# Optimization experiments

Hardware: AMD Instinct MI355X
Metric: run time of the kernel (lower is better)

Reference implementation:

```python
import jax, jax.numpy as jnp
import numpy as np

HEADS = 4
KD = 32          # key_dim per head
LEVELS = 2
G = 3            # 2**dims - 1 HP orientation groups
STRENGTH = 0.25
DECAY = 0.6
LN_EPS = 1e-5
MIX_EPS = 1e-3


def _layernorm(x, g, b):
    m = jnp.mean(x, axis=-1, keepdims=True)
    v = jnp.var(x, axis=-1, keepdims=True)
    return (x - m) * jax.lax.rsqrt(v + LN_EPS) * g + b


def _dwt2(x):
    # Haar analysis, periodic/even sizes. [B,H,W,C] -> [B,H/2,W/2,4C] (LL,LH,HL,HH)
    x00 = x[:, 0::2, 0::2]; x01 = x[:, 0::2, 1::2]
    x10 = x[:, 1::2, 0::2]; x11 = x[:, 1::2, 1::2]
    ll = (x00 + x01 + x10 + x11) * 0.5
    lh = (x00 - x01 + x10 - x11) * 0.5
    hl = (x00 + x01 - x10 - x11) * 0.5
    hh = (x00 - x01 - x10 + x11) * 0.5
    return jnp.concatenate([ll, lh, hl, hh], axis=-1)


def _idwt2(w):
    # exact Haar synthesis: [B,H/2,W/2,4C] -> [B,H,W,C]
    ll, lh, hl, hh = jnp.split(w, 4, axis=-1)
    x00 = (ll + lh + hl + hh) * 0.5
    x01 = (ll - lh + hl - hh) * 0.5
    x10 = (ll + lh - hl - hh) * 0.5
    x11 = (ll - lh - hl + hh) * 0.5
    B, H2, W2, C = ll.shape
    r0 = jnp.stack([x00, x01], axis=3).reshape(B, H2, 2 * W2, C)  # interleave W
    r1 = jnp.stack([x10, x11], axis=3).reshape(B, H2, 2 * W2, C)
    return jnp.stack([r0, r1], axis=2).reshape(B, 2 * H2, 2 * W2, C)  # interleave H


def _axial_mhsa(x, p):
    # AxialMHSAND: sequential sweep over spatial axes; each pass is
    # proj(attn(softmax(QK^T/sqrt(d)) V)) on norm(x), qkv via 1x1 conv (=matmul).
    g, b, wq, bq, wk, bk, wv, bv, wp, bp = p
    scale = KD ** -0.5
    for axis in (1, 2):
        X = _layernorm(x, g, b)
        B, H, W, _ = X.shape
        Q = (X @ wq + bq).reshape(B, H, W, HEADS, KD)
        K = (X @ wk + bk).reshape(B, H, W, HEADS, KD)
        V = (X @ wv + bv).reshape(B, H, W, HEADS, KD)
        if axis == 1:  # attend along H, batch over (B, W, heads)
            A = jax.nn.softmax(jnp.einsum('bqwnd,bkwnd->bwnqk', Q, K) * scale, axis=-1)
            Y = jnp.einsum('bwnqk,bkwnd->bqwnd', A, V)
        else:          # attend along W, batch over (B, H, heads)
            A = jax.nn.softmax(jnp.einsum('bhqnd,bhknd->bhnqk', Q, K) * scale, axis=-1)
            Y = jnp.einsum('bhnqk,bhknd->bhqnd', A, V)
        x = Y.reshape(B, H, W, HEADS * KD) @ wp + bp
    return x


def setup_inputs() -> dict:
    key = jax.random.key(0)
    ks = jax.random.split(key, 24)
    C = 64
    HD = HEADS * KD
    s = 0.02
    inp = {'x': jax.random.normal(ks[0], (4, 256, 256, C), jnp.float32)}
    i = 1
    for pre in ('lp', 'hp'):
        inp[pre + '_ln_g'] = jnp.ones((C,), jnp.float32)
        inp[pre + '_ln_b'] = jnp.zeros((C,), jnp.float32)
        inp[pre + '_wq'] = jax.random.normal(ks[i], (C, HD), jnp.float32) * s
        inp[pre + '_bq'] = jax.random.normal(ks[i + 1], (HD,), jnp.float32) * s
        inp[pre + '_wk'] = jax.random.normal(ks[i + 2], (C, HD), jnp.float32) * s
        inp[pre + '_bk'] = jax.random.normal(ks[i + 3], (HD,), jnp.float32) * s
        inp[pre + '_wv'] = jax.random.normal(ks[i + 4], (C, HD), jnp.float32) * s
        inp[pre + '_bv'] = jax.random.normal(ks[i + 5], (HD,), jnp.float32) * s
        inp[pre + '_wp'] = jax.random.normal(ks[i + 6], (HD, C), jnp.float32) * s
        inp[pre + '_bp'] = jax.random.normal(ks[i + 7], (C,), jnp.float32) * s
        i += 8
    mix = jnp.eye(G, dtype=jnp.float32) + MIX_EPS * (jnp.ones((G, G), jnp.float32) - jnp.eye(G, dtype=jnp.float32))
    inp['mix_w0'] = mix
    inp['mix_w1'] = mix
    return inp


def reference(x, lp_ln_g, lp_ln_b, lp_wq, lp_bq, lp_wk, lp_bk, lp_wv, lp_bv, lp_wp, lp_bp,
              hp_ln_g, hp_ln_b, hp_wq, hp_bq, hp_wk, hp_bk, hp_wv, hp_bv, hp_wp, hp_bp,
              mix_w0, mix_w1):
    lp_p = (lp_ln_g, lp_ln_b, lp_wq, lp_bq, lp_wk, lp_bk, lp_wv, lp_bv, lp_wp, lp_bp)
    hp_p = (hp_ln_g, hp_ln_b, hp_wq, hp_bq, hp_wk, hp_bk, hp_wv, hp_bv, hp_wp, hp_bp)
    mix_ws = [mix_w0, mix_w1]
    C = x.shape[-1]
    cur = x
    hps = []
    for _ in range(LEVELS):  # analysis pyramid
        w = _dwt2(cur)
        hps.append(w[..., C:])
        cur = w[..., :C]
    # deepest LP: axial attention, residual with full strength
    cur = cur + STRENGTH * _axial_mhsa(cur, lp_p)
    for l in reversed(range(LEVELS)):  # synthesis with per-level HP processing
        hp = hps[l]
        B, H2, W2, _ = hp.shape
        gain = STRENGTH * (DECAY ** (LEVELS - 1 - l))  # coarser levels stronger
        hp_g = hp.reshape(B, H2, W2, G, C)
        mixed = jnp.einsum('gd,bhwdc->bhwgc', mix_ws[l], hp_g)  # OrientationMix
        batched = mixed.transpose(3, 0, 1, 2, 4).reshape(G * B, H2, W2, C)
        att = _axial_mhsa(batched, hp_p)  # shared hp_attn across groups/levels
        att = att.reshape(G, B, H2, W2, C).transpose(1, 2, 3, 0, 4).reshape(B, H2, W2, G * C)
        hp_out = hp + gain * att
        cur = _idwt2(jnp.concatenate([cur, hp_out], axis=-1))
    return cur
```

## Files before the change

kernel.cpp:

```cpp
#include <hip/hip_runtime.h>

#define LN_EPS 1e-5f
#define QSCALE 0.25500526578425445f

typedef __attribute__((ext_vector_type(8))) short bf16x8;
typedef __attribute__((ext_vector_type(4))) float f32x4;

#define MFMA16(A, B, C) __builtin_amdgcn_mfma_f32_16x16x32_bf16(A, B, C, 0, 0, 0)

static __device__ __forceinline__ unsigned short f2bf_rne(float f) {
    union { unsigned int i; float f; } c; c.f = f;
    unsigned int i = c.i;
    return (unsigned short)((i + 0x7fffu + ((i >> 16) & 1u)) >> 16);
}
static __device__ __forceinline__ void bfstore2(unsigned short* p, float x, float y) {
    *(unsigned int*)p = (unsigned int)f2bf_rne(x) | ((unsigned int)f2bf_rne(y) << 16);
}
static __device__ __forceinline__ unsigned pk2(float a, float b) {
    return __builtin_amdgcn_perm(__builtin_bit_cast(unsigned, b),
                                 __builtin_bit_cast(unsigned, a), 0x07060302u);
}
static __device__ __forceinline__ unsigned short tb16(float f) {
    return (unsigned short)(__builtin_bit_cast(unsigned, f) >> 16);
}

__global__ void dwt_kernel(const float4* __restrict__ in, float4* __restrict__ ll,
                           float4* __restrict__ hp, int B, int H2, int W2) {
    const int i = blockIdx.x * blockDim.x + threadIdx.x;
    const int total = B * H2 * W2 * 16;
    if (i >= total) return;
    const int c4 = i & 15;
    int t = i >> 4;
    const int w2 = t % W2; t /= W2;
    const int h2 = t % H2;
    const int b = t / H2;
    const int W = W2 * 2;
    const size_t base = (((size_t)b * (H2 * 2) + 2 * h2) * W + 2 * w2) * 16 + c4;
    const float4 x00 = in[base];
    const float4 x01 = in[base + 16];
    const float4 x10 = in[base + (size_t)W * 16];
    const float4 x11 = in[base + (size_t)W * 16 + 16];
    float4 vll, vlh, vhl, vhh;
#define DWTC(a) \
    vll.a = (x00.a + x01.a + x10.a + x11.a) * 0.5f; \
    vlh.a = (x00.a - x01.a + x10.a - x11.a) * 0.5f; \
    vhl.a = (x00.a + x01.a - x10.a - x11.a) * 0.5f; \
    vhh.a = (x00.a - x01.a - x10.a + x11.a) * 0.5f;
    DWTC(x) DWTC(y) DWTC(z) DWTC(w)
#undef DWTC
    const size_t oi = ((size_t)b * H2 + h2) * W2 + w2;
    ll[oi * 16 + c4] = vll;
    hp[oi * 48 + c4] = vlh;
    hp[oi * 48 + 16 + c4] = vhl;
    hp[oi * 48 + 32 + c4] = vhh;
}

__global__ void idwt_kernel(const float4* __restrict__ cur, const float4* __restrict__ hp,
                            const float4* __restrict__ att, float gain,
                            float4* __restrict__ out, int B, int H2, int W2) {
    const int i = blockIdx.x * blockDim.x + threadIdx.x;
    const int total = B * H2 * W2 * 16;
    if (i >= total) return;
    const int c4 = i & 15;
    int t = i >> 4;
    const int w2 = t % W2; t /= W2;
    const int h2 = t % H2;
    const int b = t / H2;
    const size_t oi = ((size_t)b * H2 + h2) * W2 + w2;
    const size_t sp = (size_t)h2 * W2 + w2;
    const size_t gstr = (size_t)B * H2 * W2;
    const float4 vll = cur[oi * 16 + c4];
    float4 vlh = hp[oi * 48 + c4];
    float4 vhl = hp[oi * 48 + 16 + c4];
    float4 vhh = hp[oi * 48 + 32 + c4];
    const float4 a0 = att[((size_t)b * H2 * W2 + sp) * 16 + c4];
    const float4 a1 = att[((size_t)b * H2 * W2 + gstr + sp) * 16 + c4];
    const float4 a2 = att[((size_t)b * H2 * W2 + 2 * gstr + sp) * 16 + c4];
#define ADDG(a) \
    vlh.a = fmaf(gain, a0.a, vlh.a); \
    vhl.a = fmaf(gain, a1.a, vhl.a); \
    vhh.a = fmaf(gain, a2.a, vhh.a);
    ADDG(x) ADDG(y) ADDG(z) ADDG(w)
#undef ADDG
    float4 x00, x01, x10, x11;
#define IDWTC(a) \
    x00.a = (vll.a + vlh.a + vhl.a + vhh.a) * 0.5f; \
    x01.a = (vll.a - vlh.a + vhl.a - vhh.a) * 0.5f; \
    x10.a = (vll.a + vlh.a - vhl.a - vhh.a) * 0.5f; \
    x11.a = (vll.a - vlh.a - vhl.a + vhh.a) * 0.5f;
    IDWTC(x) IDWTC(y) IDWTC(z) IDWTC(w)
#undef IDWTC
    const int W = W2 * 2;
    const size_t r0 = (((size_t)b * (H2 * 2) + 2 * h2) * W + 2 * w2) * 16 + c4;
    out[r0] = x00;
    out[r0 + 16] = x01;
    out[r0 + (size_t)W * 16] = x10;
    out[r0 + (size_t)W * 16 + 16] = x11;
}

__global__ void prep_weights(const float* __restrict__ lwq, const float* __restrict__ lwk,
                             const float* __restrict__ lwv, const float* __restrict__ lwp,
                             const float* __restrict__ hwq, const float* __restrict__ hwk,
                             const float* __restrict__ hwv, const float* __restrict__ hwp,
                             unsigned short* __restrict__ wbuf) {
    const int i = blockIdx.x * blockDim.x + threadIdx.x;
    if (i >= 65536) return;
    const int set = i >> 15;
    const int r = i & 32767;
    const float* wq = set ? hwq : lwq;
    const float* wk = set ? hwk : lwk;
    const float* wv = set ? hwv : lwv;
    const float* wp = set ? hwp : lwp;
    float v;
    if (r < 24576) {
        const int nn = r >> 6, c = r & 63;
        const float* w = (nn < 128) ? wq : (nn < 256) ? wk : wv;
        v = w[c * 128 + (nn & 127)];
        if (nn < 128) v *= QSCALE;
    } else {
        const int r2 = r - 24576;
        const int nn = r2 >> 7, d = r2 & 127;
        v = wp[d * 64 + nn];
    }
    wbuf[i] = f2bf_rne(v);
}

struct Job {
    const float* xin;
    const float* mixsrc;
    const float* mixw;
    float* xout;
    const float* basep;
    float res_scale;
    const float* ln_g; const float* ln_b;
    const float* bq; const float* bk; const float* bv; const float* bp;
    const unsigned short* wqkvT;
    const unsigned short* wpT;
};

template<int S>
__global__ __launch_bounds__(S * 4, 2)
void axial_attn(Job jA, Job jB, int nA, int axis)
{
    constexpr int BS = S * 4;
    constexpr int NW = BS / 64;
    constexpr int XSTR = 72;
    constexpr int QSTR = 136;
    constexpr int PSTR = S + 8;
    constexpr int NTPW = 24 / NW;

    __shared__ __align__(16) unsigned short Xs[S * XSTR];
    __shared__ __align__(16) unsigned short Qs[S * QSTR];
    __shared__ __align__(16) unsigned short Ks[S * QSTR];
    __shared__ __align__(16) unsigned short Vt[128 * PSTR];
    __shared__ __align__(16) unsigned short Pb[NW * 16 * PSTR];

    const int tid = threadIdx.x;
    const int lane = tid & 63;
    const int w = tid >> 6;
    const int n16 = lane & 15;
    const int quad = lane >> 4;

    const bool isB = (int)blockIdx.x >= nA;
    const Job j = isB ? jB : jA;
    const int line = isB ? (int)blockIdx.x - nA : (int)blockIdx.x;
    const int lb = line / S;
    const int lr = line - lb * S;
    size_t lbase, tstr;
    if (axis == 1) { lbase = ((size_t)lb * S * S + lr) * 64; tstr = (size_t)S * 64; }
    else           { lbase = ((size_t)lb * S + lr) * (size_t)S * 64; tstr = 64; }

    {
        const int sub = tid & 15;
        const float4 g4 = ((const float4*)j.ln_g)[sub];
        const float4 be4 = ((const float4*)j.ln_b)[sub];
        const float4* x4 = (const float4*)j.xin;
        const float4* hp4 = (const float4*)j.mixsrc;
        const size_t lbase4 = lbase >> 2, tstr4 = tstr >> 2;
        float m0, m1, m2; int bimg;
        if (hp4) {
            const int g = lb >> 2;
            bimg = lb & 3;
            m0 = j.mixw[g * 3 + 0]; m1 = j.mixw[g * 3 + 1]; m2 = j.mixw[g * 3 + 2];
        }
        for (int t = (tid >> 4); t < S; t += BS / 16) {
            float4 v;
            if (hp4) {
                const int pos = (axis == 1) ? (t * S + lr) : (lr * S + t);
                const size_t hb = ((size_t)bimg * S * S + pos) * 48 + sub;
                const float4 h0 = hp4[hb];
                const float4 h1 = hp4[hb + 16];
                const float4 h2 = hp4[hb + 32];
                v.x = m0 * h0.x + m1 * h1.x + m2 * h2.x;
                v.y = m0 * h0.y + m1 * h1.y + m2 * h2.y;
                v.z = m0 * h0.z + m1 * h1.z + m2 * h2.z;
                v.w = m0 * h0.w + m1 * h1.w + m2 * h2.w;
            } else {
                v = x4[lbase4 + (size_t)t * tstr4 + sub];
            }
            float s = v.x + v.y + v.z + v.w;
            float ss = v.x * v.x + v.y * v.y + v.z * v.z + v.w * v.w;
            #pragma unroll
            for (int m = 1; m < 16; m <<= 1) {
                s += __shfl_xor(s, m);
                ss += __shfl_xor(ss, m);
            }
            const float mean = s * 0.015625f;
            const float rstd = rsqrtf(ss * 0.015625f - mean * mean + LN_EPS);
            unsigned short* xr = &Xs[t * XSTR + sub * 4];
            bfstore2(xr,     (v.x - mean) * rstd * g4.x + be4.x,
                             (v.y - mean) * rstd * g4.y + be4.y);
            bfstore2(xr + 2, (v.z - mean) * rstd * g4.z + be4.z,
                             (v.w - mean) * rstd * g4.w + be4.w);
        }
    }
    __syncthreads();

    {
        bf16x8 Bf0[NTPW], Bf1[NTPW];
        float biasv[NTPW];
        #pragma unroll
        for (int i = 0; i < NTPW; ++i) {
            const int nt = w * NTPW + i;
            const int region = nt >> 3;
            const int cbase = (nt & 7) * 16;
            const float* bias_base = (region == 0) ? j.bq : (region == 1) ? j.bk : j.bv;
            float bias = bias_base[cbase + n16];
            if (region == 0) bias *= QSCALE;
            biasv[i] = bias;
            Bf0[i] = *(const bf16x8*)&j.wqkvT[(nt * 16 + n16) * 64 + quad * 8];
            Bf1[i] = *(const bf16x8*)&j.wqkvT[(nt * 16 + n16) * 64 + 32 + quad * 8];
        }
        for (int mt = 0; mt < S / 16; ++mt) {
            const bf16x8 A0 = *(const bf16x8*)&Xs[(mt * 16 + n16) * XSTR + quad * 8];
            const bf16x8 A1 = *(const bf16x8*)&Xs[(mt * 16 + n16) * XSTR + 32 + quad * 8];
            #pragma unroll
            for (int i = 0; i < NTPW; ++i) {
                const int nt = w * NTPW + i;
                const int region = nt >> 3;
                const int cbase = (nt & 7) * 16;
                f32x4 acc = {biasv[i], biasv[i], biasv[i], biasv[i]};
                acc = MFMA16(A0, Bf0[i], acc);
                acc = MFMA16(A1, Bf1[i], acc);
                if (region < 2) {
                    unsigned short* dst = (region == 0) ? Qs : Ks;
                    const int row0 = mt * 16 + quad * 4;
                    #pragma unroll
                    for (int r = 0; r < 4; ++r)
                        dst[(row0 + r) * QSTR + cbase + n16] = tb16(acc[r]);
                } else {
                    const int d = cbase + n16;
                    *(uint2*)&Vt[d * PSTR + mt * 16 + quad * 4] =
                        make_uint2(pk2(acc[0], acc[1]), pk2(acc[2], acc[3]));
                }
            }
        }
    }
    __syncthreads();

    {
        constexpr int WPH = NW / 4;
        const int h = w / WPH;
        const int sub = w - h * WPH;
        const int hoff = h * 32;
        unsigned short* pbw = &Pb[w * 16 * PSTR];
        const bf16x8 ones = (bf16x8)(short)0x3F80;

        bf16x8 vb0[S / 32], vb1[S / 32];
        #pragma unroll
        for (int kt = 0; kt < S / 32; ++kt) {
            vb0[kt] = *(const bf16x8*)&Vt[(hoff + n16) * PSTR + kt * 32 + quad * 8];
            vb1[kt] = *(const bf16x8*)&Vt[(hoff + 16 + n16) * PSTR + kt * 32 + quad * 8];
        }
        bf16x8 ka[S / 16];
        #pragma unroll
        for (int mt = 0; mt < S / 16; ++mt)
            ka[mt] = *(const bf16x8*)&Ks[(mt * 16 + n16) * QSTR + hoff + quad * 8];

        #pragma unroll
        for (int si = 0; si < 4; ++si) {
            const int q0 = (sub * 4 + si) * 16;
            const bf16x8 qb = *(const bf16x8*)&Qs[(q0 + n16) * QSTR + hoff + quad * 8];
            #pragma unroll
            for (int mt = 0; mt < S / 16; ++mt) {
                f32x4 sc = {0.f, 0.f, 0.f, 0.f};
                sc = MFMA16(ka[mt], qb, sc);
                const float e0 = __builtin_amdgcn_exp2f(sc[0]);
                const float e1 = __builtin_amdgcn_exp2f(sc[1]);
                const float e2 = __builtin_amdgcn_exp2f(sc[2]);
                const float e3 = __builtin_amdgcn_exp2f(sc[3]);
                *(uint2*)&pbw[n16 * PSTR + mt * 16 + quad * 4] =
                    make_uint2(pk2(e0, e1), pk2(e2, e3));
            }
            f32x4 accl = {0.f, 0.f, 0.f, 0.f};
            f32x4 y0 = {0.f, 0.f, 0.f, 0.f};
            f32x4 y1 = {0.f, 0.f, 0.f, 0.f};
            #pragma unroll
            for (int kt = 0; kt < S / 32; ++kt) {
                const bf16x8 pa = *(const bf16x8*)&pbw[n16 * PSTR + kt * 32 + quad * 8];
                accl = MFMA16(pa, ones, accl);
                y0 = MFMA16(pa, vb0[kt], y0);
                y1 = MFMA16(pa, vb1[kt], y1);
            }
            #pragma unroll
            for (int r = 0; r < 4; ++r) {
                const float inv = __builtin_amdgcn_rcpf(accl[r]);
                const int row = q0 + quad * 4 + r;
                Qs[row * QSTR + hoff + n16]      = tb16(y0[r] * inv);
                Qs[row * QSTR + hoff + 16 + n16] = tb16(y1[r] * inv);
            }
        }
    }
    __syncthreads();

    {
        const int m0 = w * 16;
        bf16x8 pa[4];
        #pragma unroll
        for (int kt = 0; kt < 4; ++kt)
            pa[kt] = *(const bf16x8*)&Qs[(m0 + n16) * QSTR + kt * 32 + quad * 8];
        #pragma unroll
        for (int nt = 0; nt < 4; ++nt) {
            const float bias = j.bp[nt * 16 + n16];
            f32x4 acc = {bias, bias, bias, bias};
            #pragma unroll
            for (int kt = 0; kt < 4; ++kt) {
                const bf16x8 wb = *(const bf16x8*)&j.wpT[(nt * 16 + n16) * 128 + kt * 32 + quad * 8];
                acc = MFMA16(pa[kt], wb, acc);
            }
            #pragma unroll
            for (int r = 0; r < 4; ++r) {
                const size_t gi = lbase + (size_t)(m0 + quad * 4 + r) * tstr + nt * 16 + n16;
                float v = acc[r];
                if (j.basep) v = fmaf(j.res_scale, v, j.basep[gi]);
                j.xout[gi] = v;
            }
        }
    }
}

extern "C" void kernel_launch(void* const* d_in, const int* in_sizes, int n_in,
                              void* d_out, int out_size, void* d_ws, size_t ws_size,
                              hipStream_t stream) {
    (void)in_sizes; (void)n_in; (void)out_size; (void)ws_size;
    const float* x = (const float*)d_in[0];
    const float* P_lp[10];
    const float* P_hp[10];
    for (int i = 0; i < 10; ++i) P_lp[i] = (const float*)d_in[1 + i];
    for (int i = 0; i < 10; ++i) P_hp[i] = (const float*)d_in[11 + i];
    const float* mw0 = (const float*)d_in[21];
    const float* mw1 = (const float*)d_in[22];
    float* out = (float*)d_out;
    float* ws = (float*)d_ws;

    float* ll0 = ws;
    float* hp0 = ll0 + (size_t)4194304;
    float* t0  = hp0 + (size_t)12582912;
    float* ll1  = t0;
    float* hp1  = t0 + (size_t)1048576;
    float* ta2  = t0 + (size_t)4194304;
    float* lpta = t0 + (size_t)7340032;
    float* tb  = out;
    float* t1b = out;
    unsigned short* wbuf = (unsigned short*)(out + (size_t)13631488);

    prep_weights<<<256, 256, 0, stream>>>(
        P_lp[2], P_lp[4], P_lp[6], P_lp[8],
        P_hp[2], P_hp[4], P_hp[6], P_hp[8], wbuf);

    dwt_kernel<<<4 * 128 * 128 * 16 / 256, 256, 0, stream>>>(
        (const float4*)x, (float4*)ll0, (float4*)hp0, 4, 128, 128);
    dwt_kernel<<<4 * 64 * 64 * 16 / 256, 256, 0, stream>>>(
        (const float4*)ll0, (float4*)ll1, (float4*)hp1, 4, 64, 64);

    const unsigned short* lp_qkvT = wbuf;
    const unsigned short* lp_wpT  = wbuf + 24576;
    const unsigned short* hp_qkvT = wbuf + 32768;
    const unsigned short* hp_wpT  = wbuf + 32768 + 24576;

    auto mkjob = [](const float* xin, const float* mixsrc, const float* mixw,
                    float* xout, const float* basep, float rs,
                    const float* const* P, const unsigned short* qkvT,
                    const unsigned short* wpT) {
        Job jj;
        jj.xin = xin; jj.mixsrc = mixsrc; jj.mixw = mixw;
        jj.xout = xout; jj.basep = basep; jj.res_scale = rs;
        jj.ln_g = P[0]; jj.ln_b = P[1];
        jj.bq = P[3]; jj.bk = P[5]; jj.bv = P[7]; jj.bp = P[9];
        jj.wqkvT = qkvT; jj.wpT = wpT;
        return jj;
    };

    {
        Job a1 = mkjob(ll1, nullptr, nullptr, lpta, nullptr, 1.f, P_lp, lp_qkvT, lp_wpT);
        Job b1 = mkjob(nullptr, hp1, mw1, tb, nullptr, 1.f, P_hp, hp_qkvT, hp_wpT);
        axial_attn<64><<<1024, 256, 0, stream>>>(a1, b1, 256, 1);
        Job a2 = mkjob(lpta, nullptr, nullptr, ll1, ll1, 0.25f, P_lp, lp_qkvT, lp_wpT);
        Job b2 = mkjob(tb, nullptr, nullptr, ta2, nullptr, 1.f, P_hp, hp_qkvT, hp_wpT);
        axial_attn<64><<<1024, 256, 0, stream>>>(a2, b2, 256, 2);
    }
    idwt_kernel<<<4 * 64 * 64 * 16 / 256, 256, 0, stream>>>(
        (const float4*)ll1, (const float4*)hp1, (const float4*)ta2, 0.25f,
        (float4*)ll0, 4, 64, 64);

    {
        Job c1 = mkjob(nullptr, hp0, mw0, t1b, nullptr, 1.f, P_hp, hp_qkvT, hp_wpT);
        axial_attn<128><<<1536, 512, 0, stream>>>(c1, c1, 1536, 1);
        Job c2 = mkjob(t1b, nullptr, nullptr, t0, nullptr, 1.f, P_hp, hp_qkvT, hp_wpT);
        axial_attn<128><<<1536, 512, 0, stream>>>(c2, c2, 1536, 2);
    }
    idwt_kernel<<<4 * 128 * 128 * 16 / 256, 256, 0, stream>>>(
        (const float4*)ll0, (const float4*)hp0, (const float4*)t0, 0.15f,
        (float4*)out, 4, 128, 128);
}
```

Before: 430.9 us.

## Stream K/V in 32-row chunks with swizzled LDS to cut shared memory

The axial attention kernel now uses a fixed 512-thread block and computes K and V chunk by chunk, 32 rows at a time, interleaved with the score/exp/PV MFMA steps. Only Q stays fully resident. Unpadded XOR-swizzled layouts replace the padded Xs and Qs rows. Together these shrink the LDS footprint and allow more resident blocks per CU (launch bounds 512,4). In exchange there are two extra barriers per chunk, the K/V weight fragments are reloaded from global memory on every chunk, and the S=64 launch doubles its threads per block.

```diff
diff --git a/kernel.cpp b/kernel.cpp
--- a/kernel.cpp
+++ b/kernel.cpp
@@ -139,21 +139,22 @@
 };
 
 template<int S>
-__global__ __launch_bounds__(S * 4, 2)
+__global__ __launch_bounds__(512, 4)
 void axial_attn(Job jA, Job jB, int nA, int axis)
 {
-    constexpr int BS = S * 4;
-    constexpr int NW = BS / 64;
-    constexpr int XSTR = 72;
-    constexpr int QSTR = 136;
-    constexpr int PSTR = S + 8;
-    constexpr int NTPW = 24 / NW;
-
-    __shared__ __align__(16) unsigned short Xs[S * XSTR];
-    __shared__ __align__(16) unsigned short Qs[S * QSTR];
-    __shared__ __align__(16) unsigned short Ks[S * QSTR];
-    __shared__ __align__(16) unsigned short Vt[128 * PSTR];
-    __shared__ __align__(16) unsigned short Pb[NW * 16 * PSTR];
+    constexpr int BS = 512;
+    constexpr int NW = 8;
+    constexpr int CK = 32;
+    constexpr int NCH = S / CK;
+    constexpr int CSTR = 40;
+    constexpr int WPH = 2;
+    constexpr int NSI = (S / 16) / WPH;
+
+    __shared__ __align__(16) unsigned short Xs[S * 64];
+    __shared__ __align__(16) unsigned short Qs[S * 128];
+    __shared__ __align__(16) unsigned short Kc[CK * 128];
+    __shared__ __align__(16) unsigned short Vc[128 * CSTR];
+    __shared__ __align__(16) unsigned short Pb[NW * 16 * CSTR];
 
     const int tid = threadIdx.x;
     const int lane = tid & 63;
@@ -207,7 +208,7 @@
             }
             const float mean = s * 0.015625f;
             const float rstd = rsqrtf(ss * 0.015625f - mean * mean + LN_EPS);
-            unsigned short* xr = &Xs[t * XSTR + sub * 4];
+            unsigned short* xr = &Xs[(t << 6) + ((sub * 4) ^ ((t & 7) << 3))];
             bfstore2(xr,     (v.x - mean) * rstd * g4.x + be4.x,
                              (v.y - mean) * rstd * g4.y + be4.y);
             bfstore2(xr + 2, (v.z - mean) * rstd * g4.z + be4.z,
@@ -217,110 +218,137 @@
     __syncthreads();
 
     {
-        bf16x8 Bf0[NTPW], Bf1[NTPW];
-        float biasv[NTPW];
-        #pragma unroll
-        for (int i = 0; i < NTPW; ++i) {
-            const int nt = w * NTPW + i;
-            const int region = nt >> 3;
-            const int cbase = (nt & 7) * 16;
-            const float* bias_base = (region == 0) ? j.bq : (region == 1) ? j.bk : j.bv;
-            float bias = bias_base[cbase + n16];
-            if (region == 0) bias *= QSCALE;
-            biasv[i] = bias;
-            Bf0[i] = *(const bf16x8*)&j.wqkvT[(nt * 16 + n16) * 64 + quad * 8];
-            Bf1[i] = *(const bf16x8*)&j.wqkvT[(nt * 16 + n16) * 64 + 32 + quad * 8];
-        }
+        const int nt = w;
+        const int cbase = nt * 16;
+        const float bias = j.bq[cbase + n16] * QSCALE;
+        const bf16x8 Bf0 = *(const bf16x8*)&j.wqkvT[(nt * 16 + n16) * 64 + quad * 8];
+        const bf16x8 Bf1 = *(const bf16x8*)&j.wqkvT[(nt * 16 + n16) * 64 + 32 + quad * 8];
+        #pragma unroll
         for (int mt = 0; mt < S / 16; ++mt) {
-            const bf16x8 A0 = *(const bf16x8*)&Xs[(mt * 16 + n16) * XSTR + quad * 8];
-            const bf16x8 A1 = *(const bf16x8*)&Xs[(mt * 16 + n16) * XSTR + 32 + quad * 8];
-            #pragma unroll
-            for (int i = 0; i < NTPW; ++i) {
-                const int nt = w * NTPW + i;
-                const int region = nt >> 3;
-                const int cbase = (nt & 7) * 16;
-                f32x4 acc = {biasv[i], biasv[i], biasv[i], biasv[i]};
-                acc = MFMA16(A0, Bf0[i], acc);
-                acc = MFMA16(A1, Bf1[i], acc);
-                if (region < 2) {
-                    unsigned short* dst = (region == 0) ? Qs : Ks;
-                    const int row0 = mt * 16 + quad * 4;
-                    #pragma unroll
-                    for (int r = 0; r < 4; ++r)
-                        dst[(row0 + r) * QSTR + cbase + n16] = tb16(acc[r]);
-                } else {
-                    const int d = cbase + n16;
-                    *(uint2*)&Vt[d * PSTR + mt * 16 + quad * 4] =
-                        make_uint2(pk2(acc[0], acc[1]), pk2(acc[2], acc[3]));
-                }
-            }
-        }
-    }
-    __syncthreads();
-
-    {
-        constexpr int WPH = NW / 4;
-        const int h = w / WPH;
-        const int sub = w - h * WPH;
-        const int hoff = h * 32;
-        unsigned short* pbw = &Pb[w * 16 * PSTR];
-        const bf16x8 ones = (bf16x8)(short)0x3F80;
-
-        bf16x8 vb0[S / 32], vb1[S / 32];
-        #pragma unroll
-        for (int kt = 0; kt < S / 32; ++kt) {
-            vb0[kt] = *(const bf16x8*)&Vt[(hoff + n16) * PSTR + kt * 32 + quad * 8];
-            vb1[kt] = *(const bf16x8*)&Vt[(hoff + 16 + n16) * PSTR + kt * 32 + quad * 8];
-        }
-        bf16x8 ka[S / 16];
-        #pragma unroll
-        for (int mt = 0; mt < S / 16; ++mt)
-            ka[mt] = *(const bf16x8*)&Ks[(mt * 16 + n16) * QSTR + hoff + quad * 8];
-
-        #pragma unroll
-        for (int si = 0; si < 4; ++si) {
-            const int q0 = (sub * 4 + si) * 16;
-            const bf16x8 qb = *(const bf16x8*)&Qs[(q0 + n16) * QSTR + hoff + quad * 8];
-            #pragma unroll
-            for (int mt = 0; mt < S / 16; ++mt) {
-                f32x4 sc = {0.f, 0.f, 0.f, 0.f};
-                sc = MFMA16(ka[mt], qb, sc);
-                const float e0 = __builtin_amdgcn_exp2f(sc[0]);
-                const float e1 = __builtin_amdgcn_exp2f(sc[1]);
-                const float e2 = __builtin_amdgcn_exp2f(sc[2]);
-                const float e3 = __builtin_amdgcn_exp2f(sc[3]);
-                *(uint2*)&pbw[n16 * PSTR + mt * 16 + quad * 4] =
-                    make_uint2(pk2(e0, e1), pk2(e2, e3));
-            }
-            f32x4 accl = {0.f, 0.f, 0.f, 0.f};
-            f32x4 y0 = {0.f, 0.f, 0.f, 0.f};
-            f32x4 y1 = {0.f, 0.f, 0.f, 0.f};
-            #pragma unroll
-            for (int kt = 0; kt < S / 32; ++kt) {
-                const bf16x8 pa = *(const bf16x8*)&pbw[n16 * PSTR + kt * 32 + quad * 8];
-                accl = MFMA16(pa, ones, accl);
-                y0 = MFMA16(pa, vb0[kt], y0);
-                y1 = MFMA16(pa, vb1[kt], y1);
-            }
+            const int xr = mt * 16 + n16;
+            const int xm = (xr & 7) << 3;
+            const bf16x8 A0 = *(const bf16x8*)&Xs[(xr << 6) + ((quad * 8) ^ xm)];
+            const bf16x8 A1 = *(const bf16x8*)&Xs[(xr << 6) + ((32 + quad * 8) ^ xm)];
+            f32x4 acc = {bias, bias, bias, bias};
+            acc = MFMA16(A0, Bf0, acc);
+            acc = MFMA16(A1, Bf1, acc);
+            const int row0 = mt * 16 + quad * 4;
             #pragma unroll
             for (int r = 0; r < 4; ++r) {
-                const float inv = __builtin_amdgcn_rcpf(accl[r]);
-                const int row = q0 + quad * 4 + r;
-                Qs[row * QSTR + hoff + n16]      = tb16(y0[r] * inv);
-                Qs[row * QSTR + hoff + 16 + n16] = tb16(y1[r] * inv);
+                const int rr = row0 + r;
+                Qs[(rr << 7) + ((cbase + n16) ^ ((rr & 7) << 3))] = tb16(acc[r]);
             }
         }
     }
     __syncthreads();
 
+    const int h = w >> 1;
+    const int sub = w & 1;
+    const int hoff = h * 32;
+    unsigned short* pbw = &Pb[w * 16 * CSTR];
+    const bf16x8 ones = (bf16x8)(short)0x3F80;
+
+    bf16x8 qb[NSI];
+    #pragma unroll
+    for (int si = 0; si < NSI; ++si) {
+        const int qr = (sub * NSI + si) * 16 + n16;
+        qb[si] = *(const bf16x8*)&Qs[(qr << 7) + ((hoff + quad * 8) ^ ((qr & 7) << 3))];
+    }
+    f32x4 accl[NSI], y0[NSI], y1[NSI];
+    #pragma unroll
+    for (int si = 0; si < NSI; ++si) {
+        accl[si] = (f32x4){0.f, 0.f, 0.f, 0.f};
+        y0[si]   = (f32x4){0.f, 0.f, 0.f, 0.f};
+        y1[si]   = (f32x4){0.f, 0.f, 0.f, 0.f};
+    }
+
+    for (int kc = 0; kc < NCH; ++kc) {
+        const int k0 = kc * CK;
+        #pragma unroll
+        for (int i = 0; i < 4; ++i) {
+            const int tix = w * 4 + i;
+            const int region = tix >> 4;
+            const int rem = tix & 15;
+            const int nt = rem >> 1;
+            const int mtl = rem & 1;
+            const int wnt = 8 + region * 8 + nt;
+            const bf16x8 W0 = *(const bf16x8*)&j.wqkvT[(wnt * 16 + n16) * 64 + quad * 8];
+            const bf16x8 W1 = *(const bf16x8*)&j.wqkvT[(wnt * 16 + n16) * 64 + 32 + quad * 8];
+            const float* bb = region ? j.bv : j.bk;
+            const float bias = bb[nt * 16 + n16];
+            const int xr = k0 + mtl * 16 + n16;
+            const int xm = (xr & 7) << 3;
+            const bf16x8 A0 = *(const bf16x8*)&Xs[(xr << 6) + ((quad * 8) ^ xm)];
+            const bf16x8 A1 = *(const bf16x8*)&Xs[(xr << 6) + ((32 + quad * 8) ^ xm)];
+            f32x4 acc = {bias, bias, bias, bias};
+            acc = MFMA16(A0, W0, acc);
+            acc = MFMA16(A1, W1, acc);
+            if (region == 0) {
+                const int row0 = mtl * 16 + quad * 4;
+                #pragma unroll
+                for (int r = 0; r < 4; ++r) {
+                    const int rr = row0 + r;
+                    Kc[(rr << 7) + ((nt * 16 + n16) ^ ((rr & 7) << 3))] = tb16(acc[r]);
+                }
+            } else {
+                *(uint2*)&Vc[(nt * 16 + n16) * CSTR + mtl * 16 + quad * 4] =
+                    make_uint2(pk2(acc[0], acc[1]), pk2(acc[2], acc[3]));
+            }
+        }
+        __syncthreads();
+
+        const bf16x8 vb0 = *(const bf16x8*)&Vc[(hoff + n16) * CSTR + quad * 8];
+        const bf16x8 vb1 = *(const bf16x8*)&Vc[(hoff + 16 + n16) * CSTR + quad * 8];
+        const int km = (n16 & 7) << 3;
+        const bf16x8 ka0 = *(const bf16x8*)&Kc[(n16 << 7) + ((hoff + quad * 8) ^ km)];
+        const bf16x8 ka1 = *(const bf16x8*)&Kc[((16 + n16) << 7) + ((hoff + quad * 8) ^ km)];
+        #pragma unroll
+        for (int si = 0; si < NSI; ++si) {
+            f32x4 sc0 = {0.f, 0.f, 0.f, 0.f};
+            f32x4 sc1 = {0.f, 0.f, 0.f, 0.f};
+            sc0 = MFMA16(ka0, qb[si], sc0);
+            sc1 = MFMA16(ka1, qb[si], sc1);
+            *(uint2*)&pbw[n16 * CSTR + quad * 4] = make_uint2(
+                pk2(__builtin_amdgcn_exp2f(sc0[0]), __builtin_amdgcn_exp2f(sc0[1])),
+                pk2(__builtin_amdgcn_exp2f(sc0[2]), __builtin_amdgcn_exp2f(sc0[3])));
+            *(uint2*)&pbw[n16 * CSTR + 16 + quad * 4] = make_uint2(
+                pk2(__builtin_amdgcn_exp2f(sc1[0]), __builtin_amdgcn_exp2f(sc1[1])),
+                pk2(__builtin_amdgcn_exp2f(sc1[2]), __builtin_amdgcn_exp2f(sc1[3])));
+            const bf16x8 pa = *(const bf16x8*)&pbw[n16 * CSTR + quad * 8];
+            accl[si] = MFMA16(pa, ones, accl[si]);
+            y0[si] = MFMA16(pa, vb0, y0[si]);
+            y1[si] = MFMA16(pa, vb1, y1[si]);
+        }
+        __syncthreads();
+    }
+
+    #pragma unroll
+    for (int si = 0; si < NSI; ++si) {
+        const int q0 = (sub * NSI + si) * 16;
+        #pragma unroll
+        for (int r = 0; r < 4; ++r) {
+            const float inv = __builtin_amdgcn_rcpf(accl[si][r]);
+            const int row = q0 + quad * 4 + r;
+            const int m = (row & 7) << 3;
+            Qs[(row << 7) + ((hoff + n16) ^ m)]      = tb16(y0[si][r] * inv);
+            Qs[(row << 7) + ((hoff + 16 + n16) ^ m)] = tb16(y1[si][r] * inv);
+        }
+    }
+    __syncthreads();
+
     {
-        const int m0 = w * 16;
+        constexpr int TD = (S / 16) * 4 / NW;
+        const int mt = (w * TD) >> 2;
+        const int nt0 = (w * TD) & 3;
+        const int m0 = mt * 16;
+        const int ym = (n16 & 7) << 3;
         bf16x8 pa[4];
         #pragma unroll
         for (int kt = 0; kt < 4; ++kt)
-            pa[kt] = *(const bf16x8*)&Qs[(m0 + n16) * QSTR + kt * 32 + quad * 8];
-        #pragma unroll
-        for (int nt = 0; nt < 4; ++nt) {
+            pa[kt] = *(const bf16x8*)&Qs[((m0 + n16) << 7) + ((kt * 32 + quad * 8) ^ ym)];
+        #pragma unroll
+        for (int i = 0; i < TD; ++i) {
+            const int nt = nt0 + i;
             const float bias = j.bp[nt * 16 + n16];
             f32x4 acc = {bias, bias, bias, bias};
             #pragma unroll
@@ -394,10 +422,10 @@
     {
         Job a1 = mkjob(ll1, nullptr, nullptr, lpta, nullptr, 1.f, P_lp, lp_qkvT, lp_wpT);
         Job b1 = mkjob(nullptr, hp1, mw1, tb, nullptr, 1.f, P_hp, hp_qkvT, hp_wpT);
-        axial_attn<64><<<1024, 256, 0, stream>>>(a1, b1, 256, 1);
+        axial_attn<64><<<1024, 512, 0, stream>>>(a1, b1, 256, 1);
         Job a2 = mkjob(lpta, nullptr, nullptr, ll1, ll1, 0.25f, P_lp, lp_qkvT, lp_wpT);
         Job b2 = mkjob(tb, nullptr, nullptr, ta2, nullptr, 1.f, P_hp, hp_qkvT, hp_wpT);
-        axial_attn<64><<<1024, 256, 0, stream>>>(a2, b2, 256, 2);
+        axial_attn<64><<<1024, 512, 0, stream>>>(a2, b2, 256, 2);
     }
     idwt_kernel<<<4 * 64 * 64 * 16 / 256, 256, 0, stream>>>(
         (const float4*)ll1, (const float4*)hp1, (const float4*)ta2, 0.25f,
```

Result: slower. 452.8 us (+5.1%).
